# Kernel optimization log

Hardware: AMD Instinct MI355X
Metric: run time of the kernel (lower is better)

## Reference

```python
import jax, jax.numpy as jnp
import numpy as np
from jax import lax

N = 100000   # n_nodes
E = 600000   # n_edges (no self loops by construction)
D = 128      # hidden_dim
L = 3        # n_hops
K = 5        # tail_k_threshold


def setup_inputs() -> dict:
    key = jax.random.key(0)
    ks = jax.random.split(key, 10)
    x = jax.random.normal(ks[0], (N, D), dtype=jnp.float32)
    src = jax.random.randint(ks[1], (E,), 0, N)
    off = jax.random.randint(ks[2], (E,), 1, N)
    dst = (src + off) % N  # guarantees dst != src (self loops removed in original)
    s = 1.0 / np.sqrt(D)
    def U(k, shape):
        return jax.random.uniform(k, shape, minval=-s, maxval=s, dtype=jnp.float32)
    return {
        "x": x,
        "G1": U(ks[3], (L, D, D)), "G2": U(ks[4], (L, D, D)),
        "B1": U(ks[5], (L, D, D)), "B2": U(ks[6], (L, D, D)),
        "R": U(ks[7], (L, D)),
        "edge_src": src, "edge_dst": dst,
    }


def _lrelu(v):
    return jax.nn.leaky_relu(v, 0.2)


def reference(x, G1, G2, B1, B2, R, edge_src, edge_dst):
    # row degrees of adj (A[src, dst] = 1)
    deg = jax.ops.segment_sum(jnp.ones(E, jnp.float32), edge_src, num_segments=N)
    inv_d = jnp.where(deg > 0, 1.0 / jnp.maximum(deg, 1.0), 0.0)   # left norm D^-1 A
    inv_d1 = 1.0 / (deg + 1.0)                                      # (A+I) left norm
    inv_d2 = 1.0 / (deg + 2.0)                                      # +1 virtual node
    w0, w1, w2 = inv_d[edge_src], inv_d1[edge_src], inv_d2[edge_src]
    head_mask = deg > K

    def spmm(w_edge, h):  # (D^-1 A) @ h via gather-scale-scatter
        return jax.ops.segment_sum(w_edge[:, None] * h[edge_dst], edge_src, num_segments=N)

    def propagate(head):
        h = x
        embs = [h]
        sups = []
        for l in range(L):
            nb = spmm(w0, h)
            ft = lax.stop_gradient(h)
            nbd = lax.stop_gradient(nb)
            gamma = _lrelu(ft @ G1[l].T + nbd @ G2[l].T) + 1.0
            beta = _lrelu(ft @ B1[l].T + nbd @ B2[l].T)
            m = ft + gamma * R[l] + beta - nbd   # missing_info (Relation, ablation=0)
            sups.append(m)
            if head:
                h = spmm(w1, h) + inv_d1[:, None] * h
            else:
                h = spmm(w2, h) + inv_d2[:, None] * h + m * inv_d2[:, None]
            embs.append(h)
        emb = jnp.mean(jnp.stack(embs, 0), 0)
        sup = jnp.mean(jnp.stack(sups, 0), 0)
        return emb, sup

    emb_h, _ = propagate(True)
    emb_t, _ = propagate(False)
    node_emb = jnp.where(head_mask[:, None], emb_h, emb_t)
    return node_emb
```

## Files before the change

### kernel.cpp

```cpp
#include <hip/hip_runtime.h>

#define N_NODES 100000
#define N_EDGES 600000
#define DIM 128
#define SCAN_B 1024
#define NCHUNK 98

typedef __attribute__((ext_vector_type(4))) float f32x4;
typedef __attribute__((ext_vector_type(8))) short bf16x8;
typedef __attribute__((ext_vector_type(4))) unsigned short u16x4;
typedef __attribute__((ext_vector_type(8))) unsigned short u16x8;

__device__ __forceinline__ unsigned short f2bf(float f) {
    union { float f; unsigned u; } cv; cv.f = f;
    unsigned r = (cv.u + 0x7FFFu + ((cv.u >> 16) & 1u)) >> 16;
    return (unsigned short)r;
}
__device__ __forceinline__ float bf2f(unsigned short v) {
    union { unsigned u; float f; } c; c.u = ((unsigned)v) << 16; return c.f;
}


__global__ void k_degree(const int* __restrict__ src, int* __restrict__ degi) {
    int e = blockIdx.x * 256 + threadIdx.x;
    if (e < N_EDGES) atomicAdd(&degi[src[e]], 1);
}

__global__ void k_chunksum(const int* __restrict__ degi, int* __restrict__ bsum) {
    __shared__ int sm[SCAN_B];
    int i = blockIdx.x * SCAN_B + threadIdx.x;
    sm[threadIdx.x] = (i < N_NODES) ? degi[i] : 0;
    __syncthreads();
    for (int s = SCAN_B / 2; s > 0; s >>= 1) {
        if (threadIdx.x < (unsigned)s) sm[threadIdx.x] += sm[threadIdx.x + s];
        __syncthreads();
    }
    if (threadIdx.x == 0) bsum[blockIdx.x] = sm[0];
}

__global__ void k_scanb(int* __restrict__ bsum, int nb) {
    __shared__ int sm[128];
    int t = threadIdx.x;
    int v = (t < nb) ? bsum[t] : 0;
    sm[t] = v; __syncthreads();
    for (int s = 1; s < 128; s <<= 1) {
        int a = (t >= s) ? sm[t - s] : 0;
        __syncthreads();
        sm[t] += a;
        __syncthreads();
    }
    if (t < nb) bsum[t] = sm[t] - v;
}

__global__ void k_rowptr(const int* __restrict__ degi, const int* __restrict__ bsum,
                         int* __restrict__ rowptr, int* __restrict__ cnt,
                         float* __restrict__ inv0, float* __restrict__ inv1,
                         float* __restrict__ inv2) {
    __shared__ int sm[SCAN_B];
    int i = blockIdx.x * SCAN_B + threadIdx.x;
    int v = (i < N_NODES) ? degi[i] : 0;
    sm[threadIdx.x] = v; __syncthreads();
    for (int s = 1; s < SCAN_B; s <<= 1) {
        int a = (threadIdx.x >= (unsigned)s) ? sm[threadIdx.x - s] : 0;
        __syncthreads();
        sm[threadIdx.x] += a;
        __syncthreads();
    }
    if (i < N_NODES) {
        int excl = bsum[blockIdx.x] + sm[threadIdx.x] - v;
        rowptr[i] = excl;
        cnt[i] = excl;
        float d = (float)v;
        inv0[i] = (v > 0) ? 1.0f / d : 0.0f;
        inv1[i] = 1.0f / (d + 1.0f);
        inv2[i] = 1.0f / (d + 2.0f);
    }
}

__global__ void k_fill(const int* __restrict__ src, const int* __restrict__ dst,
                       int* __restrict__ cnt, int* __restrict__ col) {
    int e = blockIdx.x * 256 + threadIdx.x;
    if (e < N_EDGES) {
        int pos = atomicAdd(&cnt[src[e]], 1);
        col[pos] = dst[e];
    }
}

__global__ void k_pack(const float* __restrict__ G1, const float* __restrict__ G2,
                       const float* __restrict__ B1, const float* __restrict__ B2,
                       short* __restrict__ Wp) {
    int idx = blockIdx.x * 256 + threadIdx.x;
    int j = idx & 7, lane = (idx >> 3) & 63, nt = (idx >> 9) & 15, kb = (idx >> 13) & 7, l = idx >> 16;
    int k = kb * 32 + (lane >> 4) * 8 + j;
    int n = nt * 16 + (lane & 15);
    float v;
    if (n < 128) {
        v = (k < 128) ? G1[(l * 128 + n) * 128 + k] : G2[(l * 128 + n) * 128 + (k - 128)];
    } else {
        int n2 = n - 128;
        v = (k < 128) ? B1[(l * 128 + n2) * 128 + k] : B2[(l * 128 + n2) * 128 + (k - 128)];
    }
    Wp[idx] = (short)f2bf(v);
}

__global__ void k_xcast(const float* __restrict__ x, unsigned short* __restrict__ xb) {
    int i = (blockIdx.x * 256 + threadIdx.x) * 4;
    f32x4 v = *(const f32x4*)(x + i);
    unsigned short o0 = f2bf(v[0]), o1 = f2bf(v[1]), o2 = f2bf(v[2]), o3 = f2bf(v[3]);
    unsigned long long pk = (unsigned long long)o0 | ((unsigned long long)o1 << 16)
                          | ((unsigned long long)o2 << 32) | ((unsigned long long)o3 << 48);
    *(unsigned long long*)(xb + i) = pk;
}


__device__ __forceinline__ void gather4(const u16x8* __restrict__ h8,
        const int* __restrict__ col, int start, int d, int lane, float* acc) {
    int c = lane & 15;
    int base = lane & 48;
    int dd = d < 16 ? d : 16;
    int idx = (c < dd) ? col[start + c] : 0;
    int dm = d;
    int tmx = __shfl_xor(dm, 16);
    dm = dm > tmx ? dm : tmx;
    tmx = __shfl_xor(dm, 32);
    dm = dm > tmx ? dm : tmx;
    int dmain = dm < 16 ? dm : 16;
    int e = 0;
    for (; e + 2 <= dmain; e += 2) {
        int c0 = __shfl(idx, base + e, 64);
        int c1 = __shfl(idx, base + e + 1, 64);
        if (e < d) {
            u16x8 v = h8[(size_t)c0 * 16 + c];
#pragma unroll
            for (int j = 0; j < 8; ++j) acc[j] += bf2f(v[j]);
        }
        if (e + 1 < d) {
            u16x8 v = h8[(size_t)c1 * 16 + c];
#pragma unroll
            for (int j = 0; j < 8; ++j) acc[j] += bf2f(v[j]);
        }
    }
    if (e < dmain) {
        int c0 = __shfl(idx, base + e, 64);
        if (e < d) {
            u16x8 v = h8[(size_t)c0 * 16 + c];
#pragma unroll
            for (int j = 0; j < 8; ++j) acc[j] += bf2f(v[j]);
        }
        ++e;
    }
    if (dm > 16) {
        for (; e < d; ++e) {
            int c0 = col[start + e];
            u16x8 v = h8[(size_t)c0 * 16 + c];
#pragma unroll
            for (int j = 0; j < 8; ++j) acc[j] += bf2f(v[j]);
        }
    }
}

__global__ __launch_bounds__(256) void k_agg0(
    const unsigned short* __restrict__ xb, unsigned short* __restrict__ Sb,
    unsigned short* __restrict__ hA, const float* __restrict__ inv1,
    const int* __restrict__ rowptr, const int* __restrict__ degi,
    const int* __restrict__ col)
{
    int lane = threadIdx.x & 63;
    int wid = (blockIdx.x * 256 + threadIdx.x) >> 6;
    int g = lane >> 4, c = lane & 15;
    int row = wid * 4 + g;
    int start = rowptr[row], d = degi[row];
    float acc[8] = {0,0,0,0,0,0,0,0};
    gather4((const u16x8*)xb, col, start, d, lane, acc);
    u16x8 hv = ((const u16x8*)xb)[(size_t)row * 16 + c];
    float w = inv1[row];
    u16x8 so, ho;
#pragma unroll
    for (int j = 0; j < 8; ++j) {
        so[j] = f2bf(acc[j]);
        ho[j] = f2bf(w * (acc[j] + bf2f(hv[j])));
    }
    ((u16x8*)Sb)[(size_t)row * 16 + c] = so;
    ((u16x8*)hA)[(size_t)row * 16 + c] = ho;
}

__global__ __launch_bounds__(256) void k_agg_head4(
    const unsigned short* __restrict__ hsrc, unsigned short* __restrict__ hnext,
    const unsigned short* __restrict__ xb, const unsigned short* __restrict__ h1b,
    float* __restrict__ outp, const float* __restrict__ inv1,
    const int* __restrict__ rowptr, const int* __restrict__ degi,
    const int* __restrict__ col, int final_hop)
{
    int lane = threadIdx.x & 63;
    int wid = (blockIdx.x * 256 + threadIdx.x) >> 6;
    int g = lane >> 4, c = lane & 15;
    int row = wid * 4 + g;
    int start = rowptr[row], d = degi[row];
    float acc[8] = {0,0,0,0,0,0,0,0};
    gather4((const u16x8*)hsrc, col, start, d, lane, acc);
    u16x8 hv = ((const u16x8*)hsrc)[(size_t)row * 16 + c];
    float w = inv1[row];
    float hn[8];
#pragma unroll
    for (int j = 0; j < 8; ++j) hn[j] = w * (acc[j] + bf2f(hv[j]));
    if (!final_hop) {
        u16x8 ho;
#pragma unroll
        for (int j = 0; j < 8; ++j) ho[j] = f2bf(hn[j]);
        ((u16x8*)hnext)[(size_t)row * 16 + c] = ho;
    } else {
        u16x8 xv = ((const u16x8*)xb)[(size_t)row * 16 + c];
        u16x8 h1 = ((const u16x8*)h1b)[(size_t)row * 16 + c];
        f32x4 e0, e1;
#pragma unroll
        for (int j = 0; j < 4; ++j)
            e0[j] = 0.25f * (bf2f(xv[j]) + bf2f(h1[j]) + bf2f(hv[j]) + hn[j]);
#pragma unroll
        for (int j = 0; j < 4; ++j)
            e1[j] = 0.25f * (bf2f(xv[4 + j]) + bf2f(h1[4 + j]) + bf2f(hv[4 + j]) + hn[4 + j]);
        float* op = outp + (size_t)row * DIM + c * 8;
        *(f32x4*)op = e0;
        *(f32x4*)(op + 4) = e1;
    }
}

__global__ __launch_bounds__(256) void k_agg_tail4(
    const unsigned short* __restrict__ hsrc, unsigned short* __restrict__ Sb,
    const int* __restrict__ rowptr, const int* __restrict__ degi,
    const int* __restrict__ col)
{
    int lane = threadIdx.x & 63;
    int wid = (blockIdx.x * 256 + threadIdx.x) >> 6;
    int g = lane >> 4, c = lane & 15;
    int row = wid * 4 + g;
    int start = rowptr[row], d = degi[row];
    float acc[8] = {0,0,0,0,0,0,0,0};
    gather4((const u16x8*)hsrc, col, start, d, lane, acc);
    u16x8 so;
#pragma unroll
    for (int j = 0; j < 8; ++j) so[j] = f2bf(acc[j]);
    ((u16x8*)Sb)[(size_t)row * 16 + c] = so;
}

__global__ __launch_bounds__(256, 4) void k_gemm_tail(
    const unsigned short* __restrict__ hb, const unsigned short* __restrict__ Sb,
    unsigned short* __restrict__ hb_next,
    const unsigned short* __restrict__ xb, const unsigned short* __restrict__ h1b,
    float* __restrict__ outp,
    const float* __restrict__ Rl, const short* __restrict__ Wp,
    const float* __restrict__ inv0, const float* __restrict__ inv2,
    const int* __restrict__ degi, int last)
{
    int wave = threadIdx.x >> 6, lane = threadIdx.x & 63;
    int quad = lane >> 4, m16 = lane & 15;
    int r0 = blockIdx.x * 64 + wave * 16;
    int rowA = r0 + m16;
    int cA = rowA < N_NODES ? rowA : N_NODES - 1;
    float w0 = inv0[cA];
    const unsigned short* hrow = hb + (size_t)cA * DIM + quad * 8;
    const unsigned short* srow = Sb + (size_t)cA * DIM + quad * 8;
    const short* wlane = Wp + lane * 8;

    f32x4 acc[16];
    const f32x4 vz = {0.f, 0.f, 0.f, 0.f};
#pragma unroll
    for (int t = 0; t < 16; ++t) acc[t] = vz;

    {
        bf16x8 ah[4];
#pragma unroll
        for (int kb = 0; kb < 4; ++kb) ah[kb] = *(const bf16x8*)(hrow + kb * 32);
#pragma unroll
        for (int kb = 0; kb < 4; ++kb) {
#pragma unroll
            for (int nt = 0; nt < 16; ++nt) {
                bf16x8 b = *(const bf16x8*)(wlane + (kb * 16 + nt) * 512);
                acc[nt] = __builtin_amdgcn_mfma_f32_16x16x32_bf16(ah[kb], b, acc[nt], 0, 0, 0);
            }
            __builtin_amdgcn_s_barrier();
        }
    }
    {
        bf16x8 as[4];
#pragma unroll
        for (int kb = 0; kb < 4; ++kb) {
            u16x8 sv = *(const u16x8*)(srow + kb * 32);
            bf16x8 a;
#pragma unroll
            for (int j = 0; j < 8; ++j) a[j] = (short)f2bf(w0 * bf2f(sv[j]));
            as[kb] = a;
        }
#pragma unroll
        for (int kb = 0; kb < 4; ++kb) {
#pragma unroll
            for (int nt = 0; nt < 16; ++nt) {
                bf16x8 b = *(const bf16x8*)(wlane + ((kb + 4) * 16 + nt) * 512);
                acc[nt] = __builtin_amdgcn_mfma_f32_16x16x32_bf16(as[kb], b, acc[nt], 0, 0, 0);
            }
            if (kb < 3) __builtin_amdgcn_s_barrier();
        }
    }

    float Rv[8];
#pragma unroll
    for (int nt = 0; nt < 8; ++nt) Rv[nt] = Rl[nt * 16 + m16];

#pragma unroll
    for (int r = 0; r < 4; ++r) {
        int gi = r0 + quad * 4 + r;
        if (gi < N_NODES) {
            float wi0 = inv0[gi], wi2 = inv2[gi];
            const unsigned short* hE = hb + (size_t)gi * DIM + m16;
            const unsigned short* sE = Sb + (size_t)gi * DIM + m16;
            if (!last) {
                unsigned short* oE = hb_next + (size_t)gi * DIM + m16;
#pragma unroll
                for (int nt = 0; nt < 8; ++nt) {
                    float z1 = acc[nt][r], z2 = acc[nt + 8][r];
                    float h = bf2f(hE[nt * 16]);
                    float sva = bf2f(sE[nt * 16]);
                    float g = (z1 > 0.f ? z1 : 0.2f * z1) + 1.0f;
                    float be = (z2 > 0.f ? z2 : 0.2f * z2);
                    float mm = h + g * Rv[nt] + be - wi0 * sva;
                    float hn = wi2 * (sva + h + mm);
                    oE[nt * 16] = f2bf(hn);
                }
            } else if (degi[gi] <= 5) {
                const unsigned short* xE = xb + (size_t)gi * DIM + m16;
                const unsigned short* h1E = h1b + (size_t)gi * DIM + m16;
                float* oE = outp + (size_t)gi * DIM + m16;
#pragma unroll
                for (int nt = 0; nt < 8; ++nt) {
                    float z1 = acc[nt][r], z2 = acc[nt + 8][r];
                    float h = bf2f(hE[nt * 16]);
                    float sva = bf2f(sE[nt * 16]);
                    float g = (z1 > 0.f ? z1 : 0.2f * z1) + 1.0f;
                    float be = (z2 > 0.f ? z2 : 0.2f * z2);
                    float mm = h + g * Rv[nt] + be - wi0 * sva;
                    float hn = wi2 * (sva + h + mm);
                    oE[nt * 16] = 0.25f * (bf2f(xE[nt * 16]) + bf2f(h1E[nt * 16]) + h + hn);
                }
            }
        }
    }
}


extern "C" void kernel_launch(void* const* d_in, const int* in_sizes, int n_in,
                              void* d_out, int out_size, void* d_ws, size_t ws_size,
                              hipStream_t stream) {
    const float* x  = (const float*)d_in[0];
    const float* G1 = (const float*)d_in[1];
    const float* G2 = (const float*)d_in[2];
    const float* B1 = (const float*)d_in[3];
    const float* B2 = (const float*)d_in[4];
    const float* R  = (const float*)d_in[5];
    const int* esrc = (const int*)d_in[6];
    const int* edst = (const int*)d_in[7];
    float* out = (float*)d_out;

    char* base = (char*)d_ws;
    size_t off = 0;
    auto alloc = [&](size_t b) -> void* {
        void* p = base + off;
        off = (off + b + 255) & ~(size_t)255;
        return p;
    };
    int* degi   = (int*)alloc(4 * N_NODES);
    int* rowptr = (int*)alloc(4 * N_NODES);
    int* cnt    = (int*)alloc(4 * N_NODES);
    int* bsum   = (int*)alloc(4 * 256);
    int* col    = (int*)alloc(4 * N_EDGES);
    float* inv0 = (float*)alloc(4 * N_NODES);
    float* inv1 = (float*)alloc(4 * N_NODES);
    float* inv2 = (float*)alloc(4 * N_NODES);
    short* Wp   = (short*)alloc(2 * 3 * 65536);
    unsigned short* xb = (unsigned short*)alloc(2ull * N_NODES * DIM);
    unsigned short* hA = (unsigned short*)alloc(2ull * N_NODES * DIM);
    unsigned short* hB = (unsigned short*)alloc(2ull * N_NODES * DIM);
    unsigned short* tA = (unsigned short*)alloc(2ull * N_NODES * DIM);
    unsigned short* Sb = (unsigned short*)alloc(2ull * N_NODES * DIM);

    hipMemsetAsync(degi, 0, 4 * N_NODES, stream);
    k_degree<<<(N_EDGES + 255) / 256, 256, 0, stream>>>(esrc, degi);
    k_chunksum<<<NCHUNK, SCAN_B, 0, stream>>>(degi, bsum);
    k_scanb<<<1, 128, 0, stream>>>(bsum, NCHUNK);
    k_rowptr<<<NCHUNK, SCAN_B, 0, stream>>>(degi, bsum, rowptr, cnt, inv0, inv1, inv2);
    k_fill<<<(N_EDGES + 255) / 256, 256, 0, stream>>>(esrc, edst, cnt, col);
    k_pack<<<768, 256, 0, stream>>>(G1, G2, B1, B2, Wp);
    k_xcast<<<12500, 256, 0, stream>>>(x, xb);

    k_agg0<<<6250, 256, 0, stream>>>(xb, Sb, hA, inv1, rowptr, degi, col);
    k_gemm_tail<<<1563, 256, 0, stream>>>(xb, Sb, tA, xb, tA, out, R, Wp, inv0, inv2, degi, 0);

    k_agg_head4<<<6250, 256, 0, stream>>>(hA, hB, xb, hA, out, inv1, rowptr, degi, col, 0);
    k_agg_head4<<<6250, 256, 0, stream>>>(hB, hB, xb, hA, out, inv1, rowptr, degi, col, 1);

    k_agg_tail4<<<6250, 256, 0, stream>>>(tA, Sb, rowptr, degi, col);
    k_gemm_tail<<<1563, 256, 0, stream>>>(tA, Sb, hB, xb, tA, out, R + 128, Wp + 65536, inv0, inv2, degi, 0);
    k_agg_tail4<<<6250, 256, 0, stream>>>(hB, Sb, rowptr, degi, col);
    k_gemm_tail<<<1563, 256, 0, stream>>>(hB, Sb, hB, xb, tA, out, R + 256, Wp + 131072, inv0, inv2, degi, 1);
}
```

Baseline: 483.7 us.

## Make gemm_tail persistent with register-resident weight columns per wave

The fused tail GEMM becomes a persistent kernel of 512 blocks with 512 threads. Each of the 8 waves keeps its 16-column slice of the packed weights (gamma and beta halves, all 8 k-blocks) in registers and loops over 16-row tiles, so the weights are no longer re-read from global memory for every tile. The block-wide barriers go away, and each wave now computes a 16x32 output slice instead of 16x256. The trade-off is that every wave re-reads the same 16 h and S rows, giving more redundant activation loads and less MFMA work per loaded row, so the kernel may end up memory-latency bound.

Measured after the change: 536.8 us. +11.0%, slower.

```diff
diff --git a/kernel.cpp b/kernel.cpp
--- a/kernel.cpp
+++ b/kernel.cpp
@@ -242,7 +242,7 @@
     ((u16x8*)Sb)[(size_t)row * 16 + c] = so;
 }
 
-__global__ __launch_bounds__(256, 4) void k_gemm_tail(
+__global__ __launch_bounds__(512, 4) void k_gemm_tail(
     const unsigned short* __restrict__ hb, const unsigned short* __restrict__ Sb,
     unsigned short* __restrict__ hb_next,
     const unsigned short* __restrict__ xb, const unsigned short* __restrict__ h1b,
@@ -253,93 +253,63 @@
 {
     int wave = threadIdx.x >> 6, lane = threadIdx.x & 63;
     int quad = lane >> 4, m16 = lane & 15;
-    int r0 = blockIdx.x * 64 + wave * 16;
-    int rowA = r0 + m16;
-    int cA = rowA < N_NODES ? rowA : N_NODES - 1;
-    float w0 = inv0[cA];
-    const unsigned short* hrow = hb + (size_t)cA * DIM + quad * 8;
-    const unsigned short* srow = Sb + (size_t)cA * DIM + quad * 8;
-    const short* wlane = Wp + lane * 8;
-
-    f32x4 acc[16];
-    const f32x4 vz = {0.f, 0.f, 0.f, 0.f};
-#pragma unroll
-    for (int t = 0; t < 16; ++t) acc[t] = vz;
-
-    {
+
+    bf16x8 b0[8], b1[8];
+    const short* wl = Wp + lane * 8;
+#pragma unroll
+    for (int kb = 0; kb < 8; ++kb) {
+        b0[kb] = *(const bf16x8*)(wl + (kb * 16 + wave) * 512);
+        b1[kb] = *(const bf16x8*)(wl + (kb * 16 + wave + 8) * 512);
+    }
+    int col = wave * 16 + m16;
+    float Rv = Rl[col];
+
+    for (int t = blockIdx.x; t < 6250; t += 512) {
+        int rb = t * 16;
+        int rowA = rb + m16;
+        const unsigned short* hrow = hb + (size_t)rowA * DIM + quad * 8;
+        const unsigned short* srow = Sb + (size_t)rowA * DIM + quad * 8;
+        float w0 = inv0[rowA];
+
         bf16x8 ah[4];
+        u16x8 sv[4];
 #pragma unroll
         for (int kb = 0; kb < 4; ++kb) ah[kb] = *(const bf16x8*)(hrow + kb * 32);
 #pragma unroll
+        for (int kb = 0; kb < 4; ++kb) sv[kb] = *(const u16x8*)(srow + kb * 32);
+
+        f32x4 a0 = {0.f, 0.f, 0.f, 0.f}, a1 = {0.f, 0.f, 0.f, 0.f};
+#pragma unroll
         for (int kb = 0; kb < 4; ++kb) {
-#pragma unroll
-            for (int nt = 0; nt < 16; ++nt) {
-                bf16x8 b = *(const bf16x8*)(wlane + (kb * 16 + nt) * 512);
-                acc[nt] = __builtin_amdgcn_mfma_f32_16x16x32_bf16(ah[kb], b, acc[nt], 0, 0, 0);
-            }
-            __builtin_amdgcn_s_barrier();
-        }
-    }
-    {
-        bf16x8 as[4];
+            a0 = __builtin_amdgcn_mfma_f32_16x16x32_bf16(ah[kb], b0[kb], a0, 0, 0, 0);
+            a1 = __builtin_amdgcn_mfma_f32_16x16x32_bf16(ah[kb], b1[kb], a1, 0, 0, 0);
+        }
 #pragma unroll
         for (int kb = 0; kb < 4; ++kb) {
-            u16x8 sv = *(const u16x8*)(srow + kb * 32);
-            bf16x8 a;
-#pragma unroll
-            for (int j = 0; j < 8; ++j) a[j] = (short)f2bf(w0 * bf2f(sv[j]));
-            as[kb] = a;
-        }
-#pragma unroll
-        for (int kb = 0; kb < 4; ++kb) {
-#pragma unroll
-            for (int nt = 0; nt < 16; ++nt) {
-                bf16x8 b = *(const bf16x8*)(wlane + ((kb + 4) * 16 + nt) * 512);
-                acc[nt] = __builtin_amdgcn_mfma_f32_16x16x32_bf16(as[kb], b, acc[nt], 0, 0, 0);
-            }
-            if (kb < 3) __builtin_amdgcn_s_barrier();
-        }
-    }
-
-    float Rv[8];
-#pragma unroll
-    for (int nt = 0; nt < 8; ++nt) Rv[nt] = Rl[nt * 16 + m16];
-
-#pragma unroll
-    for (int r = 0; r < 4; ++r) {
-        int gi = r0 + quad * 4 + r;
-        if (gi < N_NODES) {
+            bf16x8 as;
+#pragma unroll
+            for (int j = 0; j < 8; ++j) as[j] = (short)f2bf(w0 * bf2f(sv[kb][j]));
+            a0 = __builtin_amdgcn_mfma_f32_16x16x32_bf16(as, b0[kb + 4], a0, 0, 0, 0);
+            a1 = __builtin_amdgcn_mfma_f32_16x16x32_bf16(as, b1[kb + 4], a1, 0, 0, 0);
+        }
+
+#pragma unroll
+        for (int r = 0; r < 4; ++r) {
+            int gi = rb + quad * 4 + r;
             float wi0 = inv0[gi], wi2 = inv2[gi];
-            const unsigned short* hE = hb + (size_t)gi * DIM + m16;
-            const unsigned short* sE = Sb + (size_t)gi * DIM + m16;
+            float z1 = a0[r], z2 = a1[r];
+            float h = bf2f(hb[(size_t)gi * DIM + col]);
+            float sva = bf2f(Sb[(size_t)gi * DIM + col]);
+            float g = (z1 > 0.f ? z1 : 0.2f * z1) + 1.0f;
+            float be = (z2 > 0.f ? z2 : 0.2f * z2);
+            float mm = h + g * Rv + be - wi0 * sva;
+            float hn = wi2 * (sva + h + mm);
             if (!last) {
-                unsigned short* oE = hb_next + (size_t)gi * DIM + m16;
-#pragma unroll
-                for (int nt = 0; nt < 8; ++nt) {
-                    float z1 = acc[nt][r], z2 = acc[nt + 8][r];
-                    float h = bf2f(hE[nt * 16]);
-                    float sva = bf2f(sE[nt * 16]);
-                    float g = (z1 > 0.f ? z1 : 0.2f * z1) + 1.0f;
-                    float be = (z2 > 0.f ? z2 : 0.2f * z2);
-                    float mm = h + g * Rv[nt] + be - wi0 * sva;
-                    float hn = wi2 * (sva + h + mm);
-                    oE[nt * 16] = f2bf(hn);
-                }
+                hb_next[(size_t)gi * DIM + col] = f2bf(hn);
             } else if (degi[gi] <= 5) {
-                const unsigned short* xE = xb + (size_t)gi * DIM + m16;
-                const unsigned short* h1E = h1b + (size_t)gi * DIM + m16;
-                float* oE = outp + (size_t)gi * DIM + m16;
-#pragma unroll
-                for (int nt = 0; nt < 8; ++nt) {
-                    float z1 = acc[nt][r], z2 = acc[nt + 8][r];
-                    float h = bf2f(hE[nt * 16]);
-                    float sva = bf2f(sE[nt * 16]);
-                    float g = (z1 > 0.f ? z1 : 0.2f * z1) + 1.0f;
-                    float be = (z2 > 0.f ? z2 : 0.2f * z2);
-                    float mm = h + g * Rv[nt] + be - wi0 * sva;
-                    float hn = wi2 * (sva + h + mm);
-                    oE[nt * 16] = 0.25f * (bf2f(xE[nt * 16]) + bf2f(h1E[nt * 16]) + h + hn);
-                }
+                float xv = bf2f(xb[(size_t)gi * DIM + col]);
+                float h1v = bf2f(h1b[(size_t)gi * DIM + col]);
+                outp[(size_t)gi * DIM + col] = 0.25f * (xv + h1v + h + hn);
             }
         }
     }
@@ -391,13 +361,13 @@
     k_xcast<<<12500, 256, 0, stream>>>(x, xb);
 
     k_agg0<<<6250, 256, 0, stream>>>(xb, Sb, hA, inv1, rowptr, degi, col);
-    k_gemm_tail<<<1563, 256, 0, stream>>>(xb, Sb, tA, xb, tA, out, R, Wp, inv0, inv2, degi, 0);
+    k_gemm_tail<<<512, 512, 0, stream>>>(xb, Sb, tA, xb, tA, out, R, Wp, inv0, inv2, degi, 0);
 
     k_agg_head4<<<6250, 256, 0, stream>>>(hA, hB, xb, hA, out, inv1, rowptr, degi, col, 0);
     k_agg_head4<<<6250, 256, 0, stream>>>(hB, hB, xb, hA, out, inv1, rowptr, degi, col, 1);
 
     k_agg_tail4<<<6250, 256, 0, stream>>>(tA, Sb, rowptr, degi, col);
-    k_gemm_tail<<<1563, 256, 0, stream>>>(tA, Sb, hB, xb, tA, out, R + 128, Wp + 65536, inv0, inv2, degi, 0);
+    k_gemm_tail<<<512, 512, 0, stream>>>(tA, Sb, hB, xb, tA, out, R + 128, Wp + 65536, inv0, inv2, degi, 0);
     k_agg_tail4<<<6250, 256, 0, stream>>>(hB, Sb, rowptr, degi, col);
-    k_gemm_tail<<<1563, 256, 0, stream>>>(hB, Sb, hB, xb, tA, out, R + 256, Wp + 131072, inv0, inv2, degi, 1);
-}
+    k_gemm_tail<<<512, 512, 0, stream>>>(hB, Sb, hB, xb, tA, out, R + 256, Wp + 131072, inv0, inv2, degi, 1);
+}
```
